# Kernel tuning notes

Measured on AMD Instinct MI355X. Metric: run time of the kernel, lower is better.

The kernel has to match this reference:

```python
import jax, jax.numpy as jnp
import numpy as np

B, S, E, H, V, C = 256, 20, 512, 512, 32000, 1000


def _lstm_step(x, h, c, W, U, b):
    # Keras LSTM, activation='relu', recurrent_activation='sigmoid', gate order i,f,c,o
    z = x @ W + h @ U + b  # (B, 4H)
    i, f, g, o = jnp.split(z, 4, axis=-1)
    i = jax.nn.sigmoid(i)
    f = jax.nn.sigmoid(f)
    g = jax.nn.relu(g)
    o = jax.nn.sigmoid(o)
    c_new = f * c + i * g
    h_new = o * jax.nn.relu(c_new)
    return h_new, c_new


def setup_inputs() -> dict:
    key = jax.random.key(0)
    ks = jax.random.split(key, 24)
    std = 0.05
    d_in1 = S * E + 2 * E  # flattened encoder output + word embed + speaker embed
    inp = {
        "encoded_output": jax.random.normal(ks[0], (B, S, E), jnp.float32),
        "word_embedding": jax.random.normal(ks[1], (B, E), jnp.float32),
        "h0": jax.random.normal(ks[2], (B, H), jnp.float32) * std,
        "c0": jax.random.normal(ks[3], (B, H), jnp.float32) * std,
        "speaker": jax.random.randint(ks[4], (B,), 0, C),
        "addressee": jax.random.randint(ks[5], (B,), 0, C),
        "persona_emb": jax.random.normal(ks[6], (C, E), jnp.float32) * 0.1,
        "W1": jax.random.normal(ks[7], (d_in1, 4 * H), jnp.float32) * std,
        "U1": jax.random.normal(ks[8], (H, 4 * H), jnp.float32) * std,
        "b1": jnp.zeros((4 * H,), jnp.float32),
        "W2": jax.random.normal(ks[9], (H, 4 * H), jnp.float32) * std,
        "U2": jax.random.normal(ks[10], (H, 4 * H), jnp.float32) * std,
        "b2": jnp.zeros((4 * H,), jnp.float32),
        "W3": jax.random.normal(ks[11], (H, 4 * H), jnp.float32) * std,
        "U3": jax.random.normal(ks[12], (H, 4 * H), jnp.float32) * std,
        "b3": jnp.zeros((4 * H,), jnp.float32),
        "W4": jax.random.normal(ks[13], (H, 4 * H), jnp.float32) * std,
        "U4": jax.random.normal(ks[14], (H, 4 * H), jnp.float32) * std,
        "b4": jnp.zeros((4 * H,), jnp.float32),
        "Wd": jax.random.normal(ks[15], (H, V), jnp.float32) * std,
        "bd": jnp.zeros((V,), jnp.float32),
    }
    return inp


def reference(encoded_output, word_embedding, h0, c0, speaker, addressee,
              persona_emb, W1, U1, b1, W2, U2, b2, W3, U3, b3, W4, U4, b4, Wd, bd):
    b = encoded_output.shape[0]
    # The Python double loop in the original is exactly: (B,S,E) -> (B, S*E)
    enc_flat = encoded_output.reshape(b, -1)
    speaker_embed = persona_emb[speaker]  # (B, E)
    # is_speaker=True branch: concat [flattened encoder, word embed, speaker embed]
    x = jnp.concatenate([enc_flat, word_embedding, speaker_embed], axis=-1)
    # seq length is 1, so each LSTM layer is a single cell step;
    # each layer's initial state is the previous layer's final (h, c)
    h1, c1 = _lstm_step(x, h0, c0, W1, U1, b1)
    h2, c2 = _lstm_step(h1, h1, c1, W2, U2, b2)
    h3, c3 = _lstm_step(h2, h2, c2, W3, U3, b3)
    h4, c4 = _lstm_step(h3, h3, c3, W4, U4, b4)
    probs = jax.nn.softmax(h4 @ Wd + bd, axis=-1)  # (B, V)
    return probs, (h4, c4)
```

## Files before the change

### kernel.cpp

```cpp
#include <hip/hip_runtime.h>
#include <cstdint>
#include <cmath>

typedef _Float16 f16;
typedef _Float16 f16x8 __attribute__((ext_vector_type(8)));
typedef float f32x4 __attribute__((ext_vector_type(4)));

__device__ inline void gld_lds16(const void* g, void* l) {
  __builtin_amdgcn_global_load_lds(
      (__attribute__((address_space(1))) void*)(uintptr_t)g,
      (__attribute__((address_space(3))) void*)l, 16, 0, 0);
}

__global__ __launch_bounds__(256) void build_x1_kernel(
    const float* __restrict__ enc, const float* __restrict__ word,
    const float* __restrict__ pers, const int* __restrict__ speaker,
    const float* __restrict__ h0, f16* __restrict__ X)
{
  const int b  = blockIdx.y;
  const int k2 = blockIdx.x * 256 + threadIdx.x;
  const int k  = k2 * 2;
  float v0, v1;
  if (k < 10240) {
    const float* p = enc + (long long)b * 10240 + k; v0 = p[0]; v1 = p[1];
  } else if (k < 10752) {
    const float* p = word + b * 512 + (k - 10240);   v0 = p[0]; v1 = p[1];
  } else if (k < 11264) {
    const float* p = pers + (long long)speaker[b] * 512 + (k - 10752); v0 = p[0]; v1 = p[1];
  } else {
    const float* p = h0 + b * 512 + (k - 11264);     v0 = p[0]; v1 = p[1];
  }
  union { f16 h[2]; unsigned int u; } pk;
  pk.h[0] = (f16)v0; pk.h[1] = (f16)v1;
  ((unsigned int*)X)[(long long)b * 5888 + k2] = pk.u;
}

__global__ __launch_bounds__(256, 2) void gemm_f16_pipe(
    const f16* __restrict__ A, int lda,
    const float* __restrict__ B0, const float* __restrict__ B1, int ksw, int ldb,
    void* __restrict__ Cv, int ldc, long long c_split_stride, int niter,
    int store_f16)
{
  __shared__ __align__(16) f16 Ah[2][128 * 32];
  __shared__ __align__(16) f16 Bh[2][128 * 40];

  const int tid  = threadIdx.x;
  const int lane = tid & 63;
  const int wave = tid >> 6;
  const int m0 = blockIdx.x * 128;
  const int n0 = blockIdx.y * 128;
  const int kbeg = blockIdx.z * (niter * 32);

  const int a_row16 = lane >> 2;
  const int a_ksub  = ((lane & 3) ^ ((lane >> 3) & 3)) * 8;

  const int nl0  = (tid & 63) * 2;
  const int koct = tid >> 6;

  float2 bv[8];

  auto issueB = [&](int kt) {
    const int kb = kbeg + kt * 32 + koct * 8;
    #pragma unroll
    for (int i = 0; i < 8; i++) {
      const int krow = kb + i;
      const float* bp = (krow >= ksw) ? (B1 + (long long)(krow - ksw) * ldb)
                                      : (B0 + (long long)krow * ldb);
      bv[i] = *(const float2*)(bp + n0 + nl0);
    }
  };
  auto issueA = [&](int kt) {
    const int akb = kbeg + kt * 32;
    #pragma unroll
    for (int half = 0; half < 2; half++) {
      const int rb = wave * 32 + half * 16;
      const f16* gp = A + (long long)(m0 + rb + a_row16) * lda + akb + a_ksub;
      gld_lds16((const void*)gp, (void*)&Ah[kt & 1][rb * 32]);
    }
  };
  auto writeB = [&](int kt) {
    f16x8 p0, p1;
    #pragma unroll
    for (int i = 0; i < 8; i++) { p0[i] = (f16)bv[i].x; p1[i] = (f16)bv[i].y; }
    *(f16x8*)&Bh[kt & 1][(nl0    ) * 40 + koct * 8] = p0;
    *(f16x8*)&Bh[kt & 1][(nl0 + 1) * 40 + koct * 8] = p1;
  };

  const int wm = (wave & 1) * 64;
  const int wn = (wave >> 1) * 64;
  f32x4 acc[4][4] = {};

  issueB(0); issueA(0); writeB(0);
  __syncthreads();

  for (int kt = 0; kt < niter; kt++) {
    const int buf = kt & 1;
    const bool more = (kt + 1 < niter);
    if (more) { issueB(kt + 1); issueA(kt + 1); }

    f16x8 af[4], bf[4];
    #pragma unroll
    for (int mi = 0; mi < 4; mi++) {
      const int m = wm + mi * 16 + (lane & 15);
      af[mi] = *(const f16x8*)&Ah[buf][m * 32 + (((lane >> 4) ^ ((m >> 1) & 3)) * 8)];
    }
    #pragma unroll
    for (int ni = 0; ni < 4; ni++) {
      const int n = wn + ni * 16 + (lane & 15);
      bf[ni] = *(const f16x8*)&Bh[buf][n * 40 + (lane >> 4) * 8];
    }
    #pragma unroll
    for (int mi = 0; mi < 4; mi++)
      #pragma unroll
      for (int ni = 0; ni < 4; ni++)
        acc[mi][ni] = __builtin_amdgcn_mfma_f32_16x16x32_f16(af[mi], bf[ni], acc[mi][ni], 0, 0, 0);

    if (more) writeB(kt + 1);
    __syncthreads();
  }

  if (store_f16) {
    f16* Cs = (f16*)Cv + (long long)blockIdx.z * c_split_stride;
    #pragma unroll
    for (int mi = 0; mi < 4; mi++) {
      const int r0 = m0 + wm + mi * 16 + (lane >> 4) * 4;
      #pragma unroll
      for (int ni = 0; ni < 4; ni++) {
        const int cc = n0 + wn + ni * 16 + (lane & 15);
        #pragma unroll
        for (int r = 0; r < 4; r++)
          Cs[(long long)(r0 + r) * ldc + cc] = (f16)acc[mi][ni][r];
      }
    }
  } else {
    float* Cs = (float*)Cv + (long long)blockIdx.z * c_split_stride;
    #pragma unroll
    for (int mi = 0; mi < 4; mi++) {
      const int r0 = m0 + wm + mi * 16 + (lane >> 4) * 4;
      #pragma unroll
      for (int ni = 0; ni < 4; ni++) {
        const int cc = n0 + wn + ni * 16 + (lane & 15);
        #pragma unroll
        for (int r = 0; r < 4; r++)
          Cs[(long long)(r0 + r) * ldc + cc] = acc[mi][ni][r];
      }
    }
  }
}

__global__ __launch_bounds__(256, 2) void lstm_fused_layer(
    const f16* __restrict__ A,
    const float* __restrict__ W, const float* __restrict__ U,
    const float* __restrict__ bias,
    const float* __restrict__ c_prev, float* __restrict__ c_out,
    f16* __restrict__ h16_out, float* __restrict__ h32_out)
{
  __shared__ __align__(16) f16 Ah[2][64 * 32];
  __shared__ __align__(16) f16 Bh[2][64 * 40];
  __shared__ float zx[64 * 16 * 4];

  const int tid  = threadIdx.x;
  const int lane = tid & 63;
  const int wave = tid >> 6;
  const int m0 = blockIdx.x * 64;
  const int j0 = blockIdx.y * 16;

  const int a_row4  = lane >> 2;
  const int a_ksub  = ((lane & 3) ^ ((lane >> 3) & 3)) * 8;

  const int nl   = tid & 63;
  const int ng   = (nl >> 4) * 512 + j0 + (nl & 15);
  const int koct = tid >> 6;

  float bv[8];
  auto issueB = [&](int kt) {
    const int kb = kt * 32 + koct * 8;
    #pragma unroll
    for (int i = 0; i < 8; i++) {
      const int krow = kb + i;
      const float* bp = (krow >= 512) ? (U + (long long)(krow - 512) * 2048)
                                      : (W + (long long)krow * 2048);
      bv[i] = bp[ng];
    }
  };
  auto issueA = [&](int kt) {
    const int ak = (kt * 32 + a_ksub) & 511;
    const f16* gp = A + (long long)(m0 + wave * 16 + a_row4) * 512 + ak;
    gld_lds16((const void*)gp, (void*)&Ah[kt & 1][wave * 16 * 32]);
  };
  auto writeB = [&](int kt) {
    f16x8 p;
    #pragma unroll
    for (int i = 0; i < 8; i++) p[i] = (f16)bv[i];
    *(f16x8*)&Bh[kt & 1][nl * 40 + koct * 8] = p;
  };

  f32x4 acc[4] = {};

  issueB(0); issueA(0); writeB(0);
  __syncthreads();

  for (int kt = 0; kt < 32; kt++) {
    const int buf = kt & 1;
    const bool more = (kt + 1 < 32);
    if (more) { issueB(kt + 1); issueA(kt + 1); }

    f16x8 af[4], bfr;
    #pragma unroll
    for (int mi = 0; mi < 4; mi++) {
      const int m = mi * 16 + (lane & 15);
      af[mi] = *(const f16x8*)&Ah[buf][m * 32 + (((lane >> 4) ^ ((m >> 1) & 3)) * 8)];
    }
    bfr = *(const f16x8*)&Bh[buf][(wave * 16 + (lane & 15)) * 40 + (lane >> 4) * 8];
    #pragma unroll
    for (int mi = 0; mi < 4; mi++)
      acc[mi] = __builtin_amdgcn_mfma_f32_16x16x32_f16(af[mi], bfr, acc[mi], 0, 0, 0);

    if (more) writeB(kt + 1);
    __syncthreads();
  }

  #pragma unroll
  for (int mi = 0; mi < 4; mi++) {
    const int rbase = mi * 16 + (lane >> 4) * 4;
    #pragma unroll
    for (int r = 0; r < 4; r++)
      zx[((rbase + r) * 16 + (lane & 15)) * 4 + wave] = acc[mi][r];
  }
  __syncthreads();

  #pragma unroll
  for (int i = 0; i < 4; i++) {
    const int cell = i * 256 + tid;
    const int m = cell >> 4;
    const int j = cell & 15;
    const float4 z = ((const float4*)zx)[cell];
    const float zi = z.x + bias[j0 + j];
    const float zf = z.y + bias[512 + j0 + j];
    const float zg = z.z + bias[1024 + j0 + j];
    const float zo = z.w + bias[1536 + j0 + j];
    const float gi = 1.f / (1.f + expf(-zi));
    const float gf = 1.f / (1.f + expf(-zf));
    const float gg = fmaxf(zg, 0.f);
    const float go = 1.f / (1.f + expf(-zo));
    const int idx = (m0 + m) * 512 + j0 + j;
    const float cn = gf * c_prev[idx] + gi * gg;
    const float hn = go * fmaxf(cn, 0.f);
    c_out[idx] = cn;
    h16_out[idx] = (f16)hn;
    if (h32_out) h32_out[idx] = hn;
  }
}

__global__ __launch_bounds__(256) void gate_kernel(
    const unsigned int* __restrict__ zbase, const float* __restrict__ bias,
    const float* __restrict__ c_prev, float* __restrict__ c_out,
    f16* __restrict__ h16_out)
{
  const int idx2 = blockIdx.x * 256 + threadIdx.x;
  const int b  = idx2 >> 8;
  const int j2 = idx2 & 255;
  const int j  = j2 * 2;
  float z[4][2];
  #pragma unroll
  for (int g = 0; g < 4; g++) { z[g][0] = bias[g * 512 + j]; z[g][1] = bias[g * 512 + j + 1]; }
  for (int s = 0; s < 16; s++) {
    const unsigned int* zp = zbase + s * 262144 + b * 1024;
    #pragma unroll
    for (int g = 0; g < 4; g++) {
      union { unsigned int u; f16 h[2]; } v;
      v.u = zp[g * 256 + j2];
      z[g][0] += (float)v.h[0];
      z[g][1] += (float)v.h[1];
    }
  }
  #pragma unroll
  for (int e = 0; e < 2; e++) {
    const float gi = 1.f / (1.f + expf(-z[0][e]));
    const float gf = 1.f / (1.f + expf(-z[1][e]));
    const float gg = fmaxf(z[2][e], 0.f);
    const float go = 1.f / (1.f + expf(-z[3][e]));
    const int idx = b * 512 + j + e;
    const float cn = gf * c_prev[idx] + gi * gg;
    const float hn = go * fmaxf(cn, 0.f);
    c_out[idx] = cn;
    h16_out[idx] = (f16)hn;
  }
}

__global__ __launch_bounds__(1024) void softmax_kernel(
    float* __restrict__ logits, const float* __restrict__ bd)
{
  const int row = blockIdx.x;
  const int t = threadIdx.x;
  float4* rp = (float4*)(logits + (long long)row * 32000);
  const float4* bp = (const float4*)bd;
  float4 l[8];
  float m = -1e30f;
  #pragma unroll
  for (int i = 0; i < 8; i++) {
    const int v = t + i * 1024;
    if (v < 8000) {
      float4 x = rp[v]; const float4 bb = bp[v];
      x.x += bb.x; x.y += bb.y; x.z += bb.z; x.w += bb.w;
      l[i] = x;
      m = fmaxf(m, fmaxf(fmaxf(x.x, x.y), fmaxf(x.z, x.w)));
    } else {
      l[i] = make_float4(-1e30f, -1e30f, -1e30f, -1e30f);
    }
  }
  #pragma unroll
  for (int off = 32; off > 0; off >>= 1) m = fmaxf(m, __shfl_xor(m, off, 64));
  __shared__ float redm[16];
  __shared__ float reds[16];
  const int w = t >> 6;
  if ((t & 63) == 0) redm[w] = m;
  __syncthreads();
  float bm = redm[0];
  #pragma unroll
  for (int i = 1; i < 16; i++) bm = fmaxf(bm, redm[i]);
  float s = 0.f;
  #pragma unroll
  for (int i = 0; i < 8; i++) {
    const float ex = expf(l[i].x - bm), ey = expf(l[i].y - bm);
    const float ez = expf(l[i].z - bm), ew = expf(l[i].w - bm);
    l[i] = make_float4(ex, ey, ez, ew);
    s += (ex + ey) + (ez + ew);
  }
  #pragma unroll
  for (int off = 32; off > 0; off >>= 1) s += __shfl_xor(s, off, 64);
  if ((t & 63) == 0) reds[w] = s;
  __syncthreads();
  float ts = 0.f;
  #pragma unroll
  for (int i = 0; i < 16; i++) ts += reds[i];
  const float inv = 1.0f / ts;
  #pragma unroll
  for (int i = 0; i < 8; i++) {
    const int v = t + i * 1024;
    if (v < 8000) {
      float4 x = l[i];
      x.x *= inv; x.y *= inv; x.z *= inv; x.w *= inv;
      rp[v] = x;
    }
  }
}

extern "C" void kernel_launch(void* const* d_in, const int* in_sizes, int n_in,
                              void* d_out, int out_size, void* d_ws, size_t ws_size,
                              hipStream_t stream) {
  const float* enc     = (const float*)d_in[0];
  const float* word    = (const float*)d_in[1];
  const float* h0      = (const float*)d_in[2];
  const float* c0      = (const float*)d_in[3];
  const int*   speaker = (const int*)d_in[4];
  const float* pers = (const float*)d_in[6];
  const float* W1 = (const float*)d_in[7];
  const float* U1 = (const float*)d_in[8];
  const float* b1 = (const float*)d_in[9];
  const float* W2 = (const float*)d_in[10];
  const float* U2 = (const float*)d_in[11];
  const float* b2 = (const float*)d_in[12];
  const float* W3 = (const float*)d_in[13];
  const float* U3 = (const float*)d_in[14];
  const float* b3 = (const float*)d_in[15];
  const float* W4 = (const float*)d_in[16];
  const float* U4 = (const float*)d_in[17];
  const float* b4 = (const float*)d_in[18];
  const float* Wd = (const float*)d_in[19];
  const float* bd = (const float*)d_in[20];

  float* out = (float*)d_out;
  f16*   zp16  = (f16*)d_out;
  f16*   X1h   = (f16*)((char*)d_out + 16777216);
  float* cbuf  = out + 6291456;
  float* h4_out = out + 8192000;
  float* c4_out = out + 8192000 + 131072;

  f16* hA = (f16*)d_ws;
  f16* hB = (f16*)((char*)d_ws + 262144);
  f16* hC = (f16*)((char*)d_ws + 524288);

  const int BIG = 1 << 29;

  build_x1_kernel<<<dim3(23, 256), 256, 0, stream>>>(enc, word, pers, speaker, h0, X1h);

  gemm_f16_pipe<<<dim3(2, 16, 16), 256, 0, stream>>>(
      X1h, 11776, W1, U1, 11264, 2048, zp16, 2048, 524288LL, 23, 1);
  gate_kernel<<<dim3(256), 256, 0, stream>>>((const unsigned int*)zp16, b1, c0, cbuf, hA);

  lstm_fused_layer<<<dim3(4, 32), 256, 0, stream>>>(hA, W2, U2, b2, cbuf, cbuf, hB, nullptr);
  lstm_fused_layer<<<dim3(4, 32), 256, 0, stream>>>(hB, W3, U3, b3, cbuf, cbuf, hA, nullptr);
  lstm_fused_layer<<<dim3(4, 32), 256, 0, stream>>>(hA, W4, U4, b4, cbuf, c4_out, hC, h4_out);

  gemm_f16_pipe<<<dim3(2, 250, 1), 256, 0, stream>>>(
      hC, 512, Wd, Wd, BIG, 32000, out, 32000, 0LL, 16, 0);

  softmax_kernel<<<dim3(256), 1024, 0, stream>>>(out, bd);
}
```

Measured before the change: 392.1 us.

## Fold W+U for layers 2-4 into transposed f16 weights and use small-wave LSTM kernel

```diff
diff --git a/kernel.cpp b/kernel.cpp
--- a/kernel.cpp
+++ b/kernel.cpp
@@ -35,6 +35,30 @@
   ((unsigned int*)X)[(long long)b * 5888 + k2] = pk.u;
 }
 
+__global__ __launch_bounds__(256) void wsum_t_kernel(
+    const float* __restrict__ W2, const float* __restrict__ U2,
+    const float* __restrict__ W3, const float* __restrict__ U3,
+    const float* __restrict__ W4, const float* __restrict__ U4,
+    f16* __restrict__ out)
+{
+  const int t = blockIdx.x * 256 + threadIdx.x;
+  const int L = blockIdx.y;
+  const float* W = (L == 0) ? W2 : (L == 1) ? W3 : W4;
+  const float* U = (L == 0) ? U2 : (L == 1) ? U3 : U4;
+  const int n  = t & 2047;
+  const int k0 = (t >> 11) << 6;
+  f16* op = out + (long long)L * (2048 * 512) + (long long)n * 512 + k0;
+  for (int kk = 0; kk < 64; kk += 8) {
+    f16x8 v;
+    #pragma unroll
+    for (int j = 0; j < 8; j++) {
+      const int k = k0 + kk + j;
+      v[j] = (f16)(W[(long long)k * 2048 + n] + U[(long long)k * 2048 + n]);
+    }
+    *(f16x8*)(op + kk) = v;
+  }
+}
+
 __global__ __launch_bounds__(256, 2) void gemm_f16_pipe(
     const f16* __restrict__ A, int lda,
     const float* __restrict__ B0, const float* __restrict__ B1, int ksw, int ldb,
@@ -148,107 +172,86 @@
   }
 }
 
-__global__ __launch_bounds__(256, 2) void lstm_fused_layer(
-    const f16* __restrict__ A,
-    const float* __restrict__ W, const float* __restrict__ U,
+__global__ __launch_bounds__(64) void lstm_small_layer(
+    const f16* __restrict__ h_in,
+    const f16* __restrict__ WsT,
     const float* __restrict__ bias,
     const float* __restrict__ c_prev, float* __restrict__ c_out,
     f16* __restrict__ h16_out, float* __restrict__ h32_out)
 {
-  __shared__ __align__(16) f16 Ah[2][64 * 32];
-  __shared__ __align__(16) f16 Bh[2][64 * 40];
-  __shared__ float zx[64 * 16 * 4];
-
-  const int tid  = threadIdx.x;
-  const int lane = tid & 63;
-  const int wave = tid >> 6;
-  const int m0 = blockIdx.x * 64;
-  const int j0 = blockIdx.y * 16;
-
-  const int a_row4  = lane >> 2;
-  const int a_ksub  = ((lane & 3) ^ ((lane >> 3) & 3)) * 8;
-
-  const int nl   = tid & 63;
-  const int ng   = (nl >> 4) * 512 + j0 + (nl & 15);
-  const int koct = tid >> 6;
-
-  float bv[8];
-  auto issueB = [&](int kt) {
-    const int kb = kt * 32 + koct * 8;
-    #pragma unroll
-    for (int i = 0; i < 8; i++) {
-      const int krow = kb + i;
-      const float* bp = (krow >= 512) ? (U + (long long)(krow - 512) * 2048)
-                                      : (W + (long long)krow * 2048);
-      bv[i] = bp[ng];
-    }
-  };
-  auto issueA = [&](int kt) {
-    const int ak = (kt * 32 + a_ksub) & 511;
-    const f16* gp = A + (long long)(m0 + wave * 16 + a_row4) * 512 + ak;
-    gld_lds16((const void*)gp, (void*)&Ah[kt & 1][wave * 16 * 32]);
-  };
-  auto writeB = [&](int kt) {
-    f16x8 p;
-    #pragma unroll
-    for (int i = 0; i < 8; i++) p[i] = (f16)bv[i];
-    *(f16x8*)&Bh[kt & 1][nl * 40 + koct * 8] = p;
-  };
-
-  f32x4 acc[4] = {};
-
-  issueB(0); issueA(0); writeB(0);
-  __syncthreads();
-
-  for (int kt = 0; kt < 32; kt++) {
-    const int buf = kt & 1;
-    const bool more = (kt + 1 < 32);
-    if (more) { issueB(kt + 1); issueA(kt + 1); }
-
-    f16x8 af[4], bfr;
-    #pragma unroll
-    for (int mi = 0; mi < 4; mi++) {
-      const int m = mi * 16 + (lane & 15);
-      af[mi] = *(const f16x8*)&Ah[buf][m * 32 + (((lane >> 4) ^ ((m >> 1) & 3)) * 8)];
-    }
-    bfr = *(const f16x8*)&Bh[buf][(wave * 16 + (lane & 15)) * 40 + (lane >> 4) * 8];
-    #pragma unroll
-    for (int mi = 0; mi < 4; mi++)
-      acc[mi] = __builtin_amdgcn_mfma_f32_16x16x32_f16(af[mi], bfr, acc[mi], 0, 0, 0);
-
-    if (more) writeB(kt + 1);
-    __syncthreads();
-  }
-
-  #pragma unroll
-  for (int mi = 0; mi < 4; mi++) {
-    const int rbase = mi * 16 + (lane >> 4) * 4;
-    #pragma unroll
-    for (int r = 0; r < 4; r++)
-      zx[((rbase + r) * 16 + (lane & 15)) * 4 + wave] = acc[mi][r];
-  }
-  __syncthreads();
-
-  #pragma unroll
-  for (int i = 0; i < 4; i++) {
-    const int cell = i * 256 + tid;
-    const int m = cell >> 4;
-    const int j = cell & 15;
-    const float4 z = ((const float4*)zx)[cell];
-    const float zi = z.x + bias[j0 + j];
-    const float zf = z.y + bias[512 + j0 + j];
-    const float zg = z.z + bias[1024 + j0 + j];
-    const float zo = z.w + bias[1536 + j0 + j];
-    const float gi = 1.f / (1.f + expf(-zi));
-    const float gf = 1.f / (1.f + expf(-zf));
-    const float gg = fmaxf(zg, 0.f);
-    const float go = 1.f / (1.f + expf(-zo));
-    const int idx = (m0 + m) * 512 + j0 + j;
-    const float cn = gf * c_prev[idx] + gi * gg;
-    const float hn = go * fmaxf(cn, 0.f);
-    c_out[idx] = cn;
-    h16_out[idx] = (f16)hn;
-    if (h32_out) h32_out[idx] = hn;
+  const int lane = threadIdx.x;
+  const int wid  = blockIdx.x;
+  const int jt = wid & 31, mt = wid >> 5;
+  const int m0 = mt * 32, j0 = jt * 16;
+  const int lj = lane & 15, quad = lane >> 4;
+
+  const f16* Ab = h_in + (long long)(m0 + lj) * 512 + quad * 8;
+  const f16* Bb = WsT + (long long)(j0 + lj) * 512 + quad * 8;
+  const long long GS = 512LL * 512;
+
+  f32x4 a00 = {}, a01 = {}, a02 = {}, a03 = {};
+  f32x4 a10 = {}, a11 = {}, a12 = {}, a13 = {};
+
+  f16x8 ca0 = *(const f16x8*)(Ab);
+  f16x8 ca1 = *(const f16x8*)(Ab + 16 * 512);
+  f16x8 cb0 = *(const f16x8*)(Bb);
+  f16x8 cb1 = *(const f16x8*)(Bb + GS);
+  f16x8 cb2 = *(const f16x8*)(Bb + 2 * GS);
+  f16x8 cb3 = *(const f16x8*)(Bb + 3 * GS);
+
+  #pragma unroll
+  for (int kt = 0; kt < 16; kt++) {
+    f16x8 na0 = ca0, na1 = ca1, nb0 = cb0, nb1 = cb1, nb2 = cb2, nb3 = cb3;
+    if (kt < 15) {
+      const int k = (kt + 1) * 32;
+      na0 = *(const f16x8*)(Ab + k);
+      na1 = *(const f16x8*)(Ab + 16 * 512 + k);
+      nb0 = *(const f16x8*)(Bb + k);
+      nb1 = *(const f16x8*)(Bb + GS + k);
+      nb2 = *(const f16x8*)(Bb + 2 * GS + k);
+      nb3 = *(const f16x8*)(Bb + 3 * GS + k);
+    }
+    a00 = __builtin_amdgcn_mfma_f32_16x16x32_f16(ca0, cb0, a00, 0, 0, 0);
+    a01 = __builtin_amdgcn_mfma_f32_16x16x32_f16(ca0, cb1, a01, 0, 0, 0);
+    a02 = __builtin_amdgcn_mfma_f32_16x16x32_f16(ca0, cb2, a02, 0, 0, 0);
+    a03 = __builtin_amdgcn_mfma_f32_16x16x32_f16(ca0, cb3, a03, 0, 0, 0);
+    a10 = __builtin_amdgcn_mfma_f32_16x16x32_f16(ca1, cb0, a10, 0, 0, 0);
+    a11 = __builtin_amdgcn_mfma_f32_16x16x32_f16(ca1, cb1, a11, 0, 0, 0);
+    a12 = __builtin_amdgcn_mfma_f32_16x16x32_f16(ca1, cb2, a12, 0, 0, 0);
+    a13 = __builtin_amdgcn_mfma_f32_16x16x32_f16(ca1, cb3, a13, 0, 0, 0);
+    ca0 = na0; ca1 = na1; cb0 = nb0; cb1 = nb1; cb2 = nb2; cb3 = nb3;
+  }
+
+  const float bi = bias[j0 + lj],        bfv = bias[512 + j0 + lj];
+  const float bg = bias[1024 + j0 + lj], bo  = bias[1536 + j0 + lj];
+  #pragma unroll
+  for (int r = 0; r < 4; r++) {
+    {
+      const int m = m0 + quad * 4 + r;
+      const int idx = m * 512 + j0 + lj;
+      const float gi = 1.f / (1.f + expf(-(a00[r] + bi)));
+      const float gf = 1.f / (1.f + expf(-(a01[r] + bfv)));
+      const float gg = fmaxf(a02[r] + bg, 0.f);
+      const float go = 1.f / (1.f + expf(-(a03[r] + bo)));
+      const float cn = gf * c_prev[idx] + gi * gg;
+      const float hn = go * fmaxf(cn, 0.f);
+      c_out[idx] = cn;
+      h16_out[idx] = (f16)hn;
+      if (h32_out) h32_out[idx] = hn;
+    }
+    {
+      const int m = m0 + 16 + quad * 4 + r;
+      const int idx = m * 512 + j0 + lj;
+      const float gi = 1.f / (1.f + expf(-(a10[r] + bi)));
+      const float gf = 1.f / (1.f + expf(-(a11[r] + bfv)));
+      const float gg = fmaxf(a12[r] + bg, 0.f);
+      const float go = 1.f / (1.f + expf(-(a13[r] + bo)));
+      const float cn = gf * c_prev[idx] + gi * gg;
+      const float hn = go * fmaxf(cn, 0.f);
+      c_out[idx] = cn;
+      h16_out[idx] = (f16)hn;
+      if (h32_out) h32_out[idx] = hn;
+    }
   }
 }
 
@@ -373,25 +376,28 @@
   float* out = (float*)d_out;
   f16*   zp16  = (f16*)d_out;
   f16*   X1h   = (f16*)((char*)d_out + 16777216);
-  float* cbuf  = out + 6291456;
   float* h4_out = out + 8192000;
   float* c4_out = out + 8192000 + 131072;
 
-  f16* hA = (f16*)d_ws;
-  f16* hB = (f16*)((char*)d_ws + 262144);
-  f16* hC = (f16*)((char*)d_ws + 524288);
+  f16*   hA   = (f16*)d_ws;
+  f16*   hB   = (f16*)((char*)d_ws + 262144);
+  f16*   hC   = (f16*)((char*)d_ws + 524288);
+  float* cbuf = (float*)((char*)d_ws + 786432);
+  f16*   WsT  = (f16*)((char*)d_ws + 2097152);
 
   const int BIG = 1 << 29;
+  const long long LW = 2048LL * 512;
 
   build_x1_kernel<<<dim3(23, 256), 256, 0, stream>>>(enc, word, pers, speaker, h0, X1h);
+  wsum_t_kernel<<<dim3(64, 3), 256, 0, stream>>>(W2, U2, W3, U3, W4, U4, WsT);
 
   gemm_f16_pipe<<<dim3(2, 16, 16), 256, 0, stream>>>(
       X1h, 11776, W1, U1, 11264, 2048, zp16, 2048, 524288LL, 23, 1);
   gate_kernel<<<dim3(256), 256, 0, stream>>>((const unsigned int*)zp16, b1, c0, cbuf, hA);
 
-  lstm_fused_layer<<<dim3(4, 32), 256, 0, stream>>>(hA, W2, U2, b2, cbuf, cbuf, hB, nullptr);
-  lstm_fused_layer<<<dim3(4, 32), 256, 0, stream>>>(hB, W3, U3, b3, cbuf, cbuf, hA, nullptr);
-  lstm_fused_layer<<<dim3(4, 32), 256, 0, stream>>>(hA, W4, U4, b4, cbuf, c4_out, hC, h4_out);
+  lstm_small_layer<<<dim3(256), 64, 0, stream>>>(hA, WsT,          b2, cbuf, cbuf, hB, nullptr);
+  lstm_small_layer<<<dim3(256), 64, 0, stream>>>(hB, WsT + LW,     b3, cbuf, cbuf, hA, nullptr);
+  lstm_small_layer<<<dim3(256), 64, 0, stream>>>(hA, WsT + 2 * LW, b4, cbuf, c4_out, hC, h4_out);
 
   gemm_f16_pipe<<<dim3(2, 250, 1), 256, 0, stream>>>(
       hC, 512, Wd, Wd, BIG, 32000, out, 32000, 0LL, 16, 0);
```

New measurement: 340.0 us. 1.15x faster.
